# Kernel tuning notes

Measured on AMD Instinct MI355X. Metric: run time of the kernel, lower is better.

Reference implementation:

```python
import jax, jax.numpy as jnp
import numpy as np
import math

HEAD_DIM = 64
NQ = 24          # num query heads
NKV = 4          # num kv heads
HIDDEN = 1536
WINDOW = 256     # sliding window (layer_idx=0 -> active)
THETA = 10000.0
EPS = 1e-6


def _rope(x, cos, sin):
    # x: [B,S,H,D]; cos/sin: [S,1,D//2]  (broadcast over B and heads)
    xr = x.reshape(*x.shape[:-1], -1, 2)
    x1, x2 = xr[..., 0], xr[..., 1]
    r = jnp.stack([x1 * cos - x2 * sin, x2 * cos + x1 * sin], axis=-1)
    return r.reshape(x.shape)


def setup_inputs() -> dict:
    key = jax.random.key(0)
    k1, k2, k3 = jax.random.split(key, 3)
    B, S = 2, 2048
    x = jax.random.normal(k1, (B, S, HIDDEN), dtype=jnp.float32)
    norm_scale = jnp.ones((HIDDEN,), dtype=jnp.float32)             # RMSNorm scale
    w_qkv = jax.random.normal(k2, ((NQ + 2 * NKV) * HEAD_DIM, HIDDEN), dtype=jnp.float32) * 0.02
    w_out = jax.random.normal(k3, (HIDDEN, NQ * HEAD_DIM), dtype=jnp.float32) * 0.02
    return {"x": x, "norm_scale": norm_scale, "w_qkv": w_qkv, "w_out": w_out, "start_pos": 0}


def reference(x, norm_scale, w_qkv, w_out, start_pos):
    B, S, _ = x.shape
    # RMSNorm
    var = jnp.mean(x * x, axis=-1, keepdims=True)
    xn = x * jax.lax.rsqrt(var + EPS) * norm_scale
    # QKV projection (nn.Linear: x @ W^T)
    qkv = xn @ w_qkv.T
    qs, kvs = NQ * HEAD_DIM, NKV * HEAD_DIM
    q = qkv[..., :qs].reshape(B, S, NQ, HEAD_DIM)
    k = qkv[..., qs:qs + kvs].reshape(B, S, NKV, HEAD_DIM)
    v = qkv[..., qs + kvs:].reshape(B, S, NKV, HEAD_DIM)
    # RoPE
    inv_freq = 1.0 / (THETA ** (jnp.arange(0, HEAD_DIM, 2, dtype=jnp.float32) / HEAD_DIM))
    t = jnp.arange(start_pos, start_pos + S, dtype=jnp.float32)
    freqs = t[:, None] * inv_freq[None, :]                       # [S, D//2]
    cos, sin = jnp.cos(freqs)[:, None, :], jnp.sin(freqs)[:, None, :]
    q = _rope(q, cos, sin)
    k = _rope(k, cos, sin)
    # GQA: expand kv heads (repeat_interleave over head dim)
    rep = NQ // NKV
    k = jnp.repeat(k, rep, axis=2)
    v = jnp.repeat(v, rep, axis=2)
    # attention with causal + sliding-window mask
    scale = 1.0 / math.sqrt(HEAD_DIM)
    scores = jnp.einsum('bqhd,bkhd->bhqk', q * scale, k)        # [B,H,S,S]
    ipos = start_pos + jnp.arange(S)
    j = jnp.arange(S)
    mask = (j[None, :] > ipos[:, None]) | (j[None, :] < ipos[:, None] - WINDOW)
    scores = jnp.where(mask[None, None], -jnp.inf, scores)
    probs = jax.nn.softmax(scores, axis=-1)
    attn = jnp.einsum('bhqk,bkhd->bqhd', probs, v).reshape(B, S, NQ * HEAD_DIM)
    # output projection + residual
    return x + attn @ w_out.T
```

## Files before the change

### kernel.cpp

```cpp
#include <hip/hip_runtime.h>
#include <hip/hip_bf16.h>

typedef float f32x4 __attribute__((ext_vector_type(4)));
typedef short s16x8 __attribute__((ext_vector_type(8)));
typedef unsigned short u16;

#define B_ 2
#define S_ 2048
#define HID 1536
#define NQ_ 24
#define NKV_ 4
#define HD 64
#define NTOK (B_*S_)
#define QKVN ((NQ_+2*NKV_)*HD)
#define ROPE_BLOCKS ((NTOK*28*32)/256)
#define VT_BLOCKS (B_*NKV_*(S_/64))

#define LDS_FENCE() asm volatile("" ::: "memory")

__device__ __forceinline__ float bf2f(u16 u) {
  unsigned int x = ((unsigned int)u) << 16;
  float f; __builtin_memcpy(&f, &x, 4); return f;
}
__device__ __forceinline__ u16 f2bf(float f) {
  unsigned int u; __builtin_memcpy(&u, &f, 4);
  u += 0x7fffu + ((u >> 16) & 1u);
  return (u16)(u >> 16);
}
__device__ __forceinline__ unsigned long long pk4bf(float a, float b, float c, float d) {
  __hip_bfloat162 x = __float22bfloat162_rn(make_float2(a, b));
  __hip_bfloat162 y = __float22bfloat162_rn(make_float2(c, d));
  unsigned int xi, yi;
  __builtin_memcpy(&xi, &x, 4);
  __builtin_memcpy(&yi, &y, 4);
  return (unsigned long long)xi | ((unsigned long long)yi << 32);
}

__global__ __launch_bounds__(256) void k_cvt2(const float* __restrict__ s0, int n0q,
                                              const float* __restrict__ s1, int n1q,
                                              u16* __restrict__ dst) {
  int i = blockIdx.x * 256 + threadIdx.x;
  if (i >= n0q + n1q) return;
  const float* src = (i < n0q) ? s0 : s1;
  int j = (i < n0q) ? i : i - n0q;
  f32x4 v = ((const f32x4*)src)[j];
  *(unsigned long long*)(dst + (size_t)i*4) = pk4bf(v[0], v[1], v[2], v[3]);
}

__global__ __launch_bounds__(384) void k_rmsnorm(const float* __restrict__ x,
                                                 const float* __restrict__ g,
                                                 u16* __restrict__ xn) {
  int row = blockIdx.x;
  int t = threadIdx.x;
  f32x4 v = ((const f32x4*)(x + (size_t)row * HID))[t];
  float ss = v[0]*v[0] + v[1]*v[1] + v[2]*v[2] + v[3]*v[3];
#pragma unroll
  for (int off = 1; off < 64; off <<= 1) ss += __shfl_xor(ss, off);
  __shared__ float red[6];
  if ((t & 63) == 0) red[t >> 6] = ss;
  __syncthreads();
  float tot = red[0] + red[1] + red[2] + red[3] + red[4] + red[5];
  float rs = rsqrtf(tot * (1.f/HID) + 1e-6f);
  f32x4 gv = ((const f32x4*)g)[t];
  ((unsigned long long*)(xn + (size_t)row * HID))[t] =
      pk4bf(v[0]*rs*gv[0], v[1]*rs*gv[1], v[2]*rs*gv[2], v[3]*rs*gv[3]);
}

template <bool F32OUT>
__global__ __launch_bounds__(256) void k_gemm_bt(const u16* __restrict__ A,
                                                 const u16* __restrict__ W,
                                                 void* __restrict__ Cv,
                                                 const float* __restrict__ resid,
                                                 int N, int K) {
  __shared__ __align__(16) u16 As[2][128*32];
  __shared__ __align__(16) u16 Bs[2][128*32];
  int lin = blockIdx.x;
  int xcd = lin & 7, loc = lin >> 3;
  int mloc = loc & 3, nloc = loc >> 2;
  int m0 = (xcd*4 + mloc) * 128, n0 = nloc * 128;
  int tid = threadIdx.x;
  int w = tid >> 6, l = tid & 63;
  int wr = w >> 1, wc = w & 1;
  int c = l & 15, g = l >> 4;
  f32x4 acc[4][4] = {};
  const u16* Ag = A + (size_t)(m0 + w*32 + (l>>2))*K + (l&3)*8;
  const u16* Wg = W + (size_t)(n0 + w*32 + (l>>2))*K + (l&3)*8;
  const int woff = w*32*32;
  for (int k0 = 0; k0 < K; k0 += 64) {
#pragma unroll
    for (int hf = 0; hf < 2; hf++) {
      int kk = k0 + hf*32;
      __builtin_amdgcn_global_load_lds((const __attribute__((address_space(1))) void*)(Ag + kk),
                                       (__attribute__((address_space(3))) void*)(As[hf] + woff), 16, 0, 0);
      __builtin_amdgcn_global_load_lds((const __attribute__((address_space(1))) void*)(Ag + kk + (size_t)16*K),
                                       (__attribute__((address_space(3))) void*)(As[hf] + woff + 16*32), 16, 0, 0);
      __builtin_amdgcn_global_load_lds((const __attribute__((address_space(1))) void*)(Wg + kk),
                                       (__attribute__((address_space(3))) void*)(Bs[hf] + woff), 16, 0, 0);
      __builtin_amdgcn_global_load_lds((const __attribute__((address_space(1))) void*)(Wg + kk + (size_t)16*K),
                                       (__attribute__((address_space(3))) void*)(Bs[hf] + woff + 16*32), 16, 0, 0);
    }
    __syncthreads();
#pragma unroll
    for (int hf = 0; hf < 2; hf++) {
      s16x8 af[4], bq[4];
#pragma unroll
      for (int mt = 0; mt < 4; mt++) af[mt] = *(const s16x8*)(As[hf] + (wr*64 + mt*16 + c)*32 + g*8);
#pragma unroll
      for (int nt = 0; nt < 4; nt++) bq[nt] = *(const s16x8*)(Bs[hf] + (wc*64 + nt*16 + c)*32 + g*8);
#pragma unroll
      for (int mt = 0; mt < 4; mt++)
#pragma unroll
        for (int nt = 0; nt < 4; nt++)
          acc[mt][nt] = __builtin_amdgcn_mfma_f32_16x16x32_bf16(af[mt], bq[nt], acc[mt][nt], 0, 0, 0);
    }
    __syncthreads();
  }
#pragma unroll
  for (int mt = 0; mt < 4; mt++)
#pragma unroll
    for (int nt = 0; nt < 4; nt++)
#pragma unroll
      for (int r = 0; r < 4; r++) {
        int m = m0 + wr*64 + mt*16 + g*4 + r;
        int n = n0 + wc*64 + nt*16 + c;
        size_t off = (size_t)m*N + n;
        float vv = acc[mt][nt][r];
        if (F32OUT) {
          ((float*)Cv)[off] = vv + resid[off];
        } else {
          ((u16*)Cv)[off] = f2bf(vv);
        }
      }
}

__global__ __launch_bounds__(256) void k_rope_vt(const u16* __restrict__ qkv,
                                                 u16* __restrict__ q,
                                                 u16* __restrict__ k,
                                                 u16* __restrict__ vt,
                                                 const int* __restrict__ spp) {
  __shared__ u16 tile[64][65];
  int bid = blockIdx.x;
  if (bid < ROPE_BLOCKS) {
    int idx = bid * 256 + threadIdx.x;
    int p = idx & 31;
    int h = (idx >> 5) % 28;
    int tok = idx / 896;
    int s = tok & (S_ - 1);
    int b = tok >> 11;
    float t = (float)(spp[0] + s);
    float inv = exp2f((float)p * -0.41524101186f);
    float fr = t * inv;
    float sn, cs;
    sincosf(fr, &sn, &cs);
    int col = (h < NQ_) ? h*64 + 2*p : HID + (h - NQ_)*64 + 2*p;
    unsigned int pr = *(const unsigned int*)(qkv + (size_t)tok*QKVN + col);
    float x1 = bf2f((u16)(pr & 0xffff));
    float x2 = bf2f((u16)(pr >> 16));
    float y1 = x1*cs - x2*sn;
    float y2 = x2*cs + x1*sn;
    unsigned int outp = (unsigned int)f2bf(y1) | ((unsigned int)f2bf(y2) << 16);
    if (h < NQ_) {
      *(unsigned int*)(q + (((size_t)(b*NQ_ + h))*S_ + s)*64 + 2*p) = outp;
    } else {
      *(unsigned int*)(k + (((size_t)(b*NKV_ + (h - NQ_)))*S_ + s)*64 + 2*p) = outp;
    }
  } else {
    int blk = bid - ROPE_BLOCKS;
    int st = blk & 31;
    int hk = (blk >> 5) & 3;
    int b = blk >> 7;
    int s0 = st * 64;
#pragma unroll
    for (int i = 0; i < 16; i++) {
      int ii = threadIdx.x + i*256;
      int r = ii >> 6, cc = ii & 63;
      tile[r][cc] = qkv[((size_t)(b*S_) + s0 + r)*QKVN + (NQ_+NKV_)*64 + hk*64 + cc];
    }
    __syncthreads();
#pragma unroll
    for (int i = 0; i < 16; i++) {
      int ii = threadIdx.x + i*256;
      int d = ii >> 6, s = ii & 63;
      vt[((size_t)(b*NKV_ + hk)*64 + d)*S_ + s0 + s] = tile[s][d];
    }
  }
}

__global__ __launch_bounds__(64, 3) void k_attn(const u16* __restrict__ q,
                                                const u16* __restrict__ k,
                                                const u16* __restrict__ vt,
                                                u16* __restrict__ ao,
                                                const int* __restrict__ spp) {
  __shared__ __align__(16) u16 Pt[32*72];
  int lin = blockIdx.x;
  int xcd = lin & 7, loc = lin >> 3;
  int qb = loc & 63;
  int bh = xcd * 6 + (loc >> 6);
  int h = bh % NQ_;
  int b = bh / NQ_;
  int q0 = qb * 32;
  int hk = h / (NQ_/NKV_);
  int l = threadIdx.x;
  int c = l & 15, g = l >> 4;
  int sp = spp[0];
  const u16* qptr = q + ((size_t)(b*NQ_ + h))*S_*64;
  const u16* kptr = k + ((size_t)(b*NKV_ + hk))*S_*64;
  const u16* vptr = vt + ((size_t)(b*NKV_ + hk))*64*S_;

  s16x8 qf[2][2];
#pragma unroll
  for (int qt = 0; qt < 2; qt++)
#pragma unroll
    for (int ks = 0; ks < 2; ks++)
      qf[qt][ks] = *(const s16x8*)(qptr + (size_t)(q0 + qt*16 + c)*64 + ks*32 + g*8);

  f32x4 o[4][2] = {};
  float m_run[2], l_run[2];
#pragma unroll
  for (int i = 0; i < 2; i++) { m_run[i] = -1e30f; l_run[i] = 0.f; }

  int lo = sp + q0 - 256; if (lo < 0) lo = 0;
  int hi = sp + q0 + 31;  if (hi > S_ - 1) hi = S_ - 1;
  int kt0 = lo >> 6, kt1 = hi >> 6;

  s16x8 kf[4][2];
#pragma unroll
  for (int km = 0; km < 4; km++)
#pragma unroll
    for (int ks = 0; ks < 2; ks++)
      kf[km][ks] = *(const s16x8*)(kptr + (size_t)(kt0*64 + km*16 + c)*64 + ks*32 + g*8);

  for (int kt = kt0; kt <= kt1; kt++) {
    s16x8 vf[2][4];
#pragma unroll
    for (int ks = 0; ks < 2; ks++)
#pragma unroll
      for (int dt = 0; dt < 4; dt++)
        vf[ks][dt] = *(const s16x8*)(vptr + (size_t)(dt*16 + c)*S_ + kt*64 + ks*32 + g*8);

    bool full = (kt*64 + 63 <= sp + q0) && (kt*64 >= sp + q0 - 225);
#pragma unroll
    for (int qt = 0; qt < 2; qt++) {
      f32x4 sa[4];
      __builtin_amdgcn_s_setprio(1);
#pragma unroll
      for (int km = 0; km < 4; km++) {
        f32x4 z = {};
        z = __builtin_amdgcn_mfma_f32_16x16x32_bf16(kf[km][0], qf[qt][0], z, 0, 0, 0);
        sa[km] = __builtin_amdgcn_mfma_f32_16x16x32_bf16(kf[km][1], qf[qt][1], z, 0, 0, 0);
      }
      __builtin_amdgcn_s_setprio(0);
      if (qt == 1 && kt < kt1) {
#pragma unroll
        for (int km = 0; km < 4; km++)
#pragma unroll
          for (int ks = 0; ks < 2; ks++)
            kf[km][ks] = *(const s16x8*)(kptr + (size_t)((kt+1)*64 + km*16 + c)*64 + ks*32 + g*8);
      }
      float mx = -1e30f;
      if (full) {
#pragma unroll
        for (int km = 0; km < 4; km++)
#pragma unroll
          for (int r = 0; r < 4; r++) {
            float sv = sa[km][r] * 0.125f;
            sa[km][r] = sv;
            mx = fmaxf(mx, sv);
          }
      } else {
        int pos = sp + q0 + qt*16 + c;
#pragma unroll
        for (int km = 0; km < 4; km++)
#pragma unroll
          for (int r = 0; r < 4; r++) {
            int key = kt*64 + km*16 + g*4 + r;
            float sv = sa[km][r] * 0.125f;
            sv = ((unsigned)(pos - key) <= 256u) ? sv : -1e30f;
            sa[km][r] = sv;
            mx = fmaxf(mx, sv);
          }
      }
      mx = fmaxf(mx, __shfl_xor(mx, 16));
      mx = fmaxf(mx, __shfl_xor(mx, 32));
      float mnew = fmaxf(m_run[qt], mx);
      float alpha = __expf(m_run[qt] - mnew);
      m_run[qt] = mnew;
      float rsum = 0.f;
#pragma unroll
      for (int km = 0; km < 4; km++) {
        float p0 = __expf(sa[km][0] - mnew);
        float p1 = __expf(sa[km][1] - mnew);
        float p2 = __expf(sa[km][2] - mnew);
        float p3 = __expf(sa[km][3] - mnew);
        rsum += p0 + p1 + p2 + p3;
        *(unsigned long long*)(Pt + (qt*16 + c)*72 + km*16 + g*4) = pk4bf(p0, p1, p2, p3);
      }
      rsum += __shfl_xor(rsum, 16);
      rsum += __shfl_xor(rsum, 32);
      l_run[qt] = l_run[qt]*alpha + rsum;
#pragma unroll
      for (int dt = 0; dt < 4; dt++) {
        o[dt][qt][0] *= alpha; o[dt][qt][1] *= alpha;
        o[dt][qt][2] *= alpha; o[dt][qt][3] *= alpha;
      }
    }
    LDS_FENCE();
    __builtin_amdgcn_s_setprio(1);
#pragma unroll
    for (int ks = 0; ks < 2; ks++)
#pragma unroll
      for (int qt = 0; qt < 2; qt++) {
        s16x8 pf = *(const s16x8*)(Pt + (qt*16 + c)*72 + ks*32 + g*8);
#pragma unroll
        for (int dt = 0; dt < 4; dt++)
          o[dt][qt] = __builtin_amdgcn_mfma_f32_16x16x32_bf16(vf[ks][dt], pf, o[dt][qt], 0, 0, 0);
      }
    __builtin_amdgcn_s_setprio(0);
    LDS_FENCE();
  }
#pragma unroll
  for (int qt = 0; qt < 2; qt++) {
    float inv = 1.f / l_run[qt];
    int qi = q0 + qt*16 + c;
    u16* row = ao + ((size_t)(b*S_) + qi)*HID + h*64;
#pragma unroll
    for (int dt = 0; dt < 4; dt++)
      *(unsigned long long*)(row + dt*16 + g*4) =
          pk4bf(o[dt][qt][0]*inv, o[dt][qt][1]*inv, o[dt][qt][2]*inv, o[dt][qt][3]*inv);
  }
}

extern "C" void kernel_launch(void* const* d_in, const int* in_sizes, int n_in,
                              void* d_out, int out_size, void* d_ws, size_t ws_size,
                              hipStream_t stream) {
  const float* x_f32    = (const float*)d_in[0];
  const float* g_f32    = (const float*)d_in[1];
  const float* wqkv_f32 = (const float*)d_in[2];
  const float* wout_f32 = (const float*)d_in[3];
  const int*   spp      = (const int*)d_in[4];
  char* ws = (char*)d_ws;
  u16* wqkvb = (u16*)(ws);
  u16* woutb = (u16*)(ws + 6291456);
  u16* xn    = (u16*)(ws + 11010048);
  u16* qkv   = (u16*)(ws + 23592960);
  u16* qbuf  = (u16*)(ws + 40370176);
  u16* kbuf  = (u16*)(ws + 52953088);
  u16* vtb   = (u16*)(ws + 55050240);
  u16* attn  = xn;

  const int nwq4 = QKVN*HID/4, nwo4 = HID*HID/4;
  k_cvt2<<<(nwq4 + nwo4 + 255)/256, 256, 0, stream>>>(wqkv_f32, nwq4, wout_f32, nwo4, wqkvb);
  k_rmsnorm<<<NTOK, 384, 0, stream>>>(x_f32, g_f32, xn);
  k_gemm_bt<false><<<32*(QKVN/128), 256, 0, stream>>>(xn, wqkvb, qkv, nullptr, QKVN, HID);
  k_rope_vt<<<ROPE_BLOCKS + VT_BLOCKS, 256, 0, stream>>>(qkv, qbuf, kbuf, vtb, spp);
  k_attn<<<B_*NQ_*(S_/32), 64, 0, stream>>>(qbuf, kbuf, vtb, attn, spp);
  k_gemm_bt<true><<<32*(HID/128), 256, 0, stream>>>(attn, woutb, d_out, x_f32, HID, HID);
}
```

Before: 221.9 us.

## Double-buffer GEMM K-tiles with XOR-swizzled LDS layout

```diff
diff --git a/kernel.cpp b/kernel.cpp
--- a/kernel.cpp
+++ b/kernel.cpp
@@ -72,8 +72,8 @@
                                                  void* __restrict__ Cv,
                                                  const float* __restrict__ resid,
                                                  int N, int K) {
-  __shared__ __align__(16) u16 As[2][128*32];
-  __shared__ __align__(16) u16 Bs[2][128*32];
+  __shared__ __align__(16) u16 As0[128*64], Bs0[128*64];
+  __shared__ __align__(16) u16 As1[128*64], Bs1[128*64];
   int lin = blockIdx.x;
   int xcd = lin & 7, loc = lin >> 3;
   int mloc = loc & 3, nloc = loc >> 2;
@@ -83,38 +83,59 @@
   int wr = w >> 1, wc = w & 1;
   int c = l & 15, g = l >> 4;
   f32x4 acc[4][4] = {};
-  const u16* Ag = A + (size_t)(m0 + w*32 + (l>>2))*K + (l&3)*8;
-  const u16* Wg = W + (size_t)(n0 + w*32 + (l>>2))*K + (l&3)*8;
-  const int woff = w*32*32;
-  for (int k0 = 0; k0 < K; k0 += 64) {
-#pragma unroll
-    for (int hf = 0; hf < 2; hf++) {
-      int kk = k0 + hf*32;
-      __builtin_amdgcn_global_load_lds((const __attribute__((address_space(1))) void*)(Ag + kk),
-                                       (__attribute__((address_space(3))) void*)(As[hf] + woff), 16, 0, 0);
-      __builtin_amdgcn_global_load_lds((const __attribute__((address_space(1))) void*)(Ag + kk + (size_t)16*K),
-                                       (__attribute__((address_space(3))) void*)(As[hf] + woff + 16*32), 16, 0, 0);
-      __builtin_amdgcn_global_load_lds((const __attribute__((address_space(1))) void*)(Wg + kk),
-                                       (__attribute__((address_space(3))) void*)(Bs[hf] + woff), 16, 0, 0);
-      __builtin_amdgcn_global_load_lds((const __attribute__((address_space(1))) void*)(Wg + kk + (size_t)16*K),
-                                       (__attribute__((address_space(3))) void*)(Bs[hf] + woff + 16*32), 16, 0, 0);
-    }
+  int r8 = l >> 3;
+  int sslot = (l & 7) ^ r8;
+  const u16* Ag = A + (size_t)(m0 + w*32 + r8)*K + sslot*8;
+  const u16* Wg = W + (size_t)(n0 + w*32 + r8)*K + sslot*8;
+
+#define STAGE(dA, dB, k0) do {                                                          \
+  _Pragma("unroll")                                                                     \
+  for (int i = 0; i < 4; i++) {                                                         \
+    __builtin_amdgcn_global_load_lds(                                                   \
+        (const __attribute__((address_space(1))) void*)(Ag + (size_t)(i*8)*K + (k0)),   \
+        (__attribute__((address_space(3))) void*)(dA + (w*32 + i*8)*64), 16, 0, 0);     \
+    __builtin_amdgcn_global_load_lds(                                                   \
+        (const __attribute__((address_space(1))) void*)(Wg + (size_t)(i*8)*K + (k0)),   \
+        (__attribute__((address_space(3))) void*)(dB + (w*32 + i*8)*64), 16, 0, 0);     \
+  } } while (0)
+
+#define COMPUTE(sA, sB) do {                                                            \
+  _Pragma("unroll")                                                                     \
+  for (int ks = 0; ks < 2; ks++) {                                                      \
+    s16x8 af[4], bq[4];                                                                 \
+    int sl = ((ks*4 + g) ^ (c & 7)) * 8;                                                \
+    _Pragma("unroll")                                                                   \
+    for (int mt = 0; mt < 4; mt++)                                                      \
+      af[mt] = *(const s16x8*)(sA + (wr*64 + mt*16 + c)*64 + sl);                       \
+    _Pragma("unroll")                                                                   \
+    for (int nt = 0; nt < 4; nt++)                                                      \
+      bq[nt] = *(const s16x8*)(sB + (wc*64 + nt*16 + c)*64 + sl);                       \
+    _Pragma("unroll")                                                                   \
+    for (int mt = 0; mt < 4; mt++)                                                      \
+      _Pragma("unroll")                                                                 \
+      for (int nt = 0; nt < 4; nt++)                                                    \
+        acc[mt][nt] = __builtin_amdgcn_mfma_f32_16x16x32_bf16(af[mt], bq[nt],           \
+                                                              acc[mt][nt], 0, 0, 0);    \
+  } } while (0)
+
+  const int NT = K >> 6;
+  STAGE(As0, Bs0, 0);
+  __syncthreads();
+  for (int t = 0; t + 2 < NT; t += 2) {
+    STAGE(As1, Bs1, (t+1)*64);
+    COMPUTE(As0, Bs0);
     __syncthreads();
-#pragma unroll
-    for (int hf = 0; hf < 2; hf++) {
-      s16x8 af[4], bq[4];
-#pragma unroll
-      for (int mt = 0; mt < 4; mt++) af[mt] = *(const s16x8*)(As[hf] + (wr*64 + mt*16 + c)*32 + g*8);
-#pragma unroll
-      for (int nt = 0; nt < 4; nt++) bq[nt] = *(const s16x8*)(Bs[hf] + (wc*64 + nt*16 + c)*32 + g*8);
-#pragma unroll
-      for (int mt = 0; mt < 4; mt++)
-#pragma unroll
-        for (int nt = 0; nt < 4; nt++)
-          acc[mt][nt] = __builtin_amdgcn_mfma_f32_16x16x32_bf16(af[mt], bq[nt], acc[mt][nt], 0, 0, 0);
-    }
+    STAGE(As0, Bs0, (t+2)*64);
+    COMPUTE(As1, Bs1);
     __syncthreads();
   }
+  STAGE(As1, Bs1, (NT-1)*64);
+  COMPUTE(As0, Bs0);
+  __syncthreads();
+  COMPUTE(As1, Bs1);
+#undef STAGE
+#undef COMPUTE
+
 #pragma unroll
   for (int mt = 0; mt < 4; mt++)
 #pragma unroll
```

After: 205.9 us. 1.08x faster.
